# Kernel tuning notes

Measured on AMD Instinct MI355X. Metric: run time of the kernel, lower is better.

## Reference

```python
import jax, jax.numpy as jnp
import numpy as np

B, C_IN, H, W = 4, 256, 32, 32
NH, DK, DV, C_OUT = 8, 256, 256, 512
DKH = DK // NH
DVH = DV // NH


def _rel_to_abs(x):
    # x: [b, n, L, 2L-1] -> [b, n, L, L] via the pad/reshape skewing trick
    b, n, L, _ = x.shape
    x = jnp.pad(x, ((0, 0), (0, 0), (0, 0), (0, 1)))          # [b,n,L,2L]
    flat = x.reshape(b, n, L * 2 * L)
    flat = jnp.pad(flat, ((0, 0), (0, 0), (0, L - 1)))
    final = flat.reshape(b, n, L + 1, 2 * L - 1)
    return final[:, :, :L, L - 1:]


def _relative_logits_1d(q5, rel_k, Hq, Wq, perm):
    # q5: [b, nh, dkh, Hq, Wq]; rel_k: [2*Wq-1, dkh]
    b = q5.shape[0]
    rel = jnp.einsum('bhdxy,md->bhxym', q5, rel_k)            # [b,nh,Hq,Wq,2Wq-1]
    rel = rel.reshape(b, NH * Hq, Wq, 2 * Wq - 1)
    rel = _rel_to_abs(rel)                                     # [b,nh*Hq,Wq,Wq]
    rel = rel.reshape(b, NH, Hq, Wq, Wq)
    rel = jnp.broadcast_to(rel[:, :, :, None], (b, NH, Hq, Hq, Wq, Wq))
    rel = jnp.transpose(rel, perm)                             # -> [b,nh,H,W,H,W]
    return rel.reshape(b, NH, Hq * Wq, Hq * Wq)


def _forward(x, w_qkv, b_qkv, w_attn, b_attn, w_out, b_out, key_rel_h, key_rel_w):
    b = x.shape[0]
    L = H * W
    # 1x1 conv projections expressed as einsum
    qkv = jnp.einsum('bchw,oc->bohw', x, w_qkv) + b_qkv[None, :, None, None]
    q, k, v = qkv[:, :DK], qkv[:, DK:2 * DK], qkv[:, 2 * DK:]
    q = q.reshape(b, NH, DKH, L) * (DKH ** -0.5)
    k = k.reshape(b, NH, DKH, L)
    v = v.reshape(b, NH, DVH, L)
    logits = jnp.einsum('bhdl,bhdm->bhlm', q, k)              # [b,nh,L,L]
    q5 = q.reshape(b, NH, DKH, H, W)
    rel_w = _relative_logits_1d(q5, key_rel_w, H, W, (0, 1, 2, 4, 3, 5))
    rel_h = _relative_logits_1d(jnp.transpose(q5, (0, 1, 2, 4, 3)),
                                key_rel_h, W, H, (0, 1, 4, 2, 5, 3))
    logits = logits + rel_h + rel_w
    weights = jax.nn.softmax(logits, axis=-1)
    attn = jnp.einsum('bhlm,bhdm->bhdl', weights, v).reshape(b, DV, H, W)
    attn = jnp.einsum('bchw,oc->bohw', attn, w_attn) + b_attn[None, :, None, None]
    conv_out = jnp.einsum('bchw,oc->bohw', x, w_out) + b_out[None, :, None, None]
    return jnp.concatenate([conv_out, attn], axis=1)          # [b, C_OUT, H, W]


def setup_inputs() -> dict:
    key = jax.random.key(0)
    ks = jax.random.split(key, 6)
    s = 0.05
    return {
        'x': jax.random.normal(ks[0], (B, C_IN, H, W), jnp.float32),
        'w_qkv': jax.random.normal(ks[1], (2 * DK + DV, C_IN), jnp.float32) * s,
        'b_qkv': jnp.zeros((2 * DK + DV,), jnp.float32),
        'w_attn': jax.random.normal(ks[2], (DV, DV), jnp.float32) * s,
        'b_attn': jnp.zeros((DV,), jnp.float32),
        'w_out': jax.random.normal(ks[3], (C_OUT - DV, C_IN), jnp.float32) * s,
        'b_out': jnp.zeros((C_OUT - DV,), jnp.float32),
        'key_rel_h': jax.random.normal(ks[4], (2 * H - 1, DKH), jnp.float32) * s,
        'key_rel_w': jax.random.normal(ks[5], (2 * W - 1, DKH), jnp.float32) * s,
    }


def reference(x, w_qkv, b_qkv, w_attn, b_attn, w_out, b_out, key_rel_h, key_rel_w):
    return _forward(x, w_qkv, b_qkv, w_attn, b_attn, w_out, b_out,
                    key_rel_h, key_rel_w)
```

## Files before the change

### kernel.cpp

```cpp
#include <hip/hip_runtime.h>

#define NB   4
#define CIN  256
#define L    1024
#define NH   8
#define DH   32
#define COUT 512

typedef _Float16 half8 __attribute__((ext_vector_type(8)));
typedef _Float16 half4 __attribute__((ext_vector_type(4)));
typedef float    f32x4 __attribute__((ext_vector_type(4)));

__global__ __launch_bounds__(256) void k_prep(const float* __restrict__ x, const float* __restrict__ wq,
                                              const float* __restrict__ wa, const float* __restrict__ wo,
                                              const float* __restrict__ krh, const float* __restrict__ krw,
                                              _Float16* __restrict__ xbT, _Float16* __restrict__ wqb,
                                              _Float16* __restrict__ wab, _Float16* __restrict__ wob,
                                              _Float16* __restrict__ wrel) {
    int blk = blockIdx.x;
    if (blk < 128) {
        __shared__ _Float16 T[32][264];
        int b  = blk >> 5;
        int ct = (blk >> 2) & 7;
        int lt = blk & 3;
        int c0 = ct * 32, l0 = lt * 256;
        int t = threadIdx.x;
        int wv = t >> 6, lane = t & 63;
        const float* xp = x + (size_t)b * CIN * L + l0;
        #pragma unroll
        for (int i = 0; i < 8; ++i) {
            int c = wv * 8 + i;
            float4 v = *(const float4*)(xp + (size_t)(c0 + c) * L + lane * 4);
            half4 h;
            h[0] = (_Float16)v.x; h[1] = (_Float16)v.y; h[2] = (_Float16)v.z; h[3] = (_Float16)v.w;
            *(half4*)&T[c][lane * 4] = h;
        }
        __syncthreads();
        _Float16* op = xbT + ((size_t)(b * L + l0 + t)) * CIN + c0;
        half8 o[4];
        #pragma unroll
        for (int i = 0; i < 32; ++i) ((_Float16*)o)[i] = T[i][t];
        #pragma unroll
        for (int v = 0; v < 4; ++v) *(half8*)(op + v * 8) = o[v];
    } else {
        int idx = (blk - 128) * 256 + threadIdx.x;
        int i4 = idx * 4;
        if (i4 < 768 * 256) {
            float4 v = *(const float4*)(wq + i4);
            half4 h; h[0] = (_Float16)v.x; h[1] = (_Float16)v.y; h[2] = (_Float16)v.z; h[3] = (_Float16)v.w;
            *(half4*)(wqb + i4) = h;
        }
        if (i4 < 256 * 256) {
            float4 va = *(const float4*)(wa + i4);
            half4 ha; ha[0] = (_Float16)va.x; ha[1] = (_Float16)va.y; ha[2] = (_Float16)va.z; ha[3] = (_Float16)va.w;
            *(half4*)(wab + i4) = ha;
            float4 vo = *(const float4*)(wo + i4);
            half4 ho; ho[0] = (_Float16)vo.x; ho[1] = (_Float16)vo.y; ho[2] = (_Float16)vo.z; ho[3] = (_Float16)vo.w;
            *(half4*)(wob + i4) = ho;
        }
        if (idx < 4096) {
            int half_sel = idx >> 11;
            int j = idx & 2047;
            float v = 0.f;
            if (j < 63 * 32) v = half_sel ? krw[j] : krh[j];
            wrel[idx] = (_Float16)v;
        }
    }
}

__global__ __launch_bounds__(256) void k_qkv(const _Float16* __restrict__ xbT, const _Float16* __restrict__ wqb,
                                             const float* __restrict__ bqkv,
                                             _Float16* __restrict__ qb, _Float16* __restrict__ kb,
                                             _Float16* __restrict__ vt) {
    int lane = threadIdx.x & 63, wv = threadIdx.x >> 6;
    int wid = blockIdx.x * 4 + wv;
    int b = wid / 768; int rem = wid - b * 768;
    int ot = rem >> 5, lt = rem & 31;
    int g = lane >> 4, q15 = lane & 15;
    int o0 = ot * 32, l0 = lt * 32;
    const _Float16* A0 = wqb + (size_t)(o0 + q15) * CIN + g * 8;
    const _Float16* B0 = xbT + ((size_t)(b * L + l0 + q15)) * CIN + g * 8;
    f32x4 acc00 = {0,0,0,0}, acc01 = {0,0,0,0}, acc10 = {0,0,0,0}, acc11 = {0,0,0,0};
    #pragma unroll
    for (int c0 = 0; c0 < CIN; c0 += 32) {
        half8 a0 = *(const half8*)(A0 + c0);
        half8 a1 = *(const half8*)(A0 + 16 * CIN + c0);
        half8 b0 = *(const half8*)(B0 + c0);
        half8 b1 = *(const half8*)(B0 + 16 * CIN + c0);
        acc00 = __builtin_amdgcn_mfma_f32_16x16x32_f16(a0, b0, acc00, 0, 0, 0);
        acc01 = __builtin_amdgcn_mfma_f32_16x16x32_f16(a0, b1, acc01, 0, 0, 0);
        acc10 = __builtin_amdgcn_mfma_f32_16x16x32_f16(a1, b0, acc10, 0, 0, 0);
        acc11 = __builtin_amdgcn_mfma_f32_16x16x32_f16(a1, b1, acc11, 0, 0, 0);
    }
    #pragma unroll
    for (int ai = 0; ai < 2; ++ai) {
        int obase = o0 + ai * 16 + 4 * g;
        float bs0 = bqkv[obase], bs1 = bqkv[obase + 1], bs2 = bqkv[obase + 2], bs3 = bqkv[obase + 3];
        #pragma unroll
        for (int bj = 0; bj < 2; ++bj) {
            f32x4 a = (ai == 0) ? (bj == 0 ? acc00 : acc01) : (bj == 0 ? acc10 : acc11);
            float av[4] = {a[0] + bs0, a[1] + bs1, a[2] + bs2, a[3] + bs3};
            int l = l0 + bj * 16 + q15;
            if (obase < 256) {
                int h = obase >> 5, d0 = obase & 31;
                half4 w;
                #pragma unroll
                for (int r = 0; r < 4; ++r) w[r] = (_Float16)(av[r] * 0.17677669529663689f);
                *(half4*)(qb + ((size_t)((b * NH + h) * L + l)) * DH + d0) = w;
            } else if (obase < 512) {
                int o = obase - 256; int h = o >> 5, d0 = o & 31;
                half4 w;
                #pragma unroll
                for (int r = 0; r < 4; ++r) w[r] = (_Float16)av[r];
                *(half4*)(kb + ((size_t)((b * NH + h) * L + l)) * DH + d0) = w;
            } else {
                int o = obase - 512; int h = o >> 5, d0 = o & 31;
                #pragma unroll
                for (int r = 0; r < 4; ++r)
                    vt[((size_t)((b * NH + h) * DH + d0 + r)) * L + l] = (_Float16)av[r];
            }
        }
    }
}

__global__ __launch_bounds__(256) void k_attn(const _Float16* __restrict__ qb, const _Float16* __restrict__ kb,
                                              const _Float16* __restrict__ vt, const _Float16* __restrict__ wrel,
                                              _Float16* __restrict__ attnT) {
    __shared__ float SM[4][576];
    __shared__ float RelS[128 * 16];
    int lane = threadIdx.x & 63, wv = threadIdx.x >> 6;
    int wid = blockIdx.x;
    int bh = wid >> 6;
    int qbase = (wid & 63) << 4;
    int g = lane >> 4, q15 = lane & 15;
    int l = qbase + q15;
    int rl = qbase >> 5;
    int cl = (qbase & 31) + q15;

    half8 bq = *(const half8*)(qb + ((size_t)(bh * L + l)) * DH + g * 8);
    const f32x4 zf = {0.f, 0.f, 0.f, 0.f};

    #pragma unroll
    for (int s = 0; s < 2; ++s) {
        int rr0 = 32 * wv + 16 * s;
        half8 wa = *(const half8*)(wrel + (rr0 + q15) * DH + g * 8);
        f32x4 rc = __builtin_amdgcn_mfma_f32_16x16x32_f16(wa, bq, zf, 0, 0, 0);
        #pragma unroll
        for (int r = 0; r < 4; ++r) RelS[(rr0 + 4 * g + r) * 16 + q15] = rc[r];
    }
    __syncthreads();

    float rw0[4], rw1[4];
    #pragma unroll
    for (int r = 0; r < 4; ++r) {
        rw0[r] = RelS[(95 + 4 * g + r - cl) * 16 + q15] - 4.0f;
        rw1[r] = RelS[(111 + 4 * g + r - cl) * 16 + q15] - 4.0f;
    }

    const _Float16* kbase = kb + (size_t)bh * L * DH;
    const _Float16* vbase = vt + (size_t)bh * DH * L;

    float l_run = 0.f;
    f32x4 o0 = {0.f, 0.f, 0.f, 0.f}, o1 = {0.f, 0.f, 0.f, 0.f};
    _Float16* plw = (_Float16*)&SM[wv][0] + q15 * 40;
    const _Float16* plr = (_Float16*)&SM[wv][0] + q15 * 40 + g * 8;

    for (int ch = wv * 8; ch < wv * 8 + 8; ++ch) {
        int m0 = ch * 32;
        half8 k0 = *(const half8*)(kbase + (size_t)(m0 + q15) * DH + g * 8);
        half8 k1 = *(const half8*)(kbase + (size_t)(m0 + 16 + q15) * DH + g * 8);
        f32x4 s0 = __builtin_amdgcn_mfma_f32_16x16x32_f16(k0, bq, zf, 0, 0, 0);
        f32x4 s1 = __builtin_amdgcn_mfma_f32_16x16x32_f16(k1, bq, zf, 0, 0, 0);
        float rh = RelS[(ch + 31 - rl) * 16 + q15];
        half4 w0, w1;
        #pragma unroll
        for (int r = 0; r < 4; ++r) {
            float p0 = __expf(s0[r] + rh + rw0[r]);
            float p1 = __expf(s1[r] + rh + rw1[r]);
            l_run += p0 + p1;
            w0[r] = (_Float16)p0;
            w1[r] = (_Float16)p1;
        }
        *(half4*)(plw + 4 * g) = w0;
        *(half4*)(plw + 16 + 4 * g) = w1;
        half8 pf = *(const half8*)plr;
        half8 v0 = *(const half8*)(vbase + (size_t)q15 * L + m0 + g * 8);
        half8 v1 = *(const half8*)(vbase + (size_t)(16 + q15) * L + m0 + g * 8);
        o0 = __builtin_amdgcn_mfma_f32_16x16x32_f16(v0, pf, o0, 0, 0, 0);
        o1 = __builtin_amdgcn_mfma_f32_16x16x32_f16(v1, pf, o1, 0, 0, 0);
    }
    l_run += __shfl_xor(l_run, 16, 64);
    l_run += __shfl_xor(l_run, 32, 64);

    float* cw = &SM[wv][lane * 9];
    cw[0] = l_run;
    #pragma unroll
    for (int r = 0; r < 4; ++r) { cw[1 + r] = o0[r]; cw[5 + r] = o1[r]; }
    __syncthreads();
    if (wv == 0) {
        float lsum = 0.f;
        float O[8];
        #pragma unroll
        for (int j = 0; j < 8; ++j) O[j] = 0.f;
        #pragma unroll
        for (int i = 0; i < 4; ++i) {
            const float* cr = &SM[i][lane * 9];
            lsum += cr[0];
            #pragma unroll
            for (int j = 0; j < 8; ++j) O[j] += cr[1 + j];
        }
        float inv = 1.f / lsum;
        int b = bh >> 3, h = bh & 7;
        _Float16* op = attnT + ((size_t)(b * L + l)) * CIN + h * DH;
        half4 e0, e1;
        #pragma unroll
        for (int r = 0; r < 4; ++r) { e0[r] = (_Float16)(O[r] * inv); e1[r] = (_Float16)(O[4 + r] * inv); }
        *(half4*)(op + 4 * g) = e0;
        *(half4*)(op + 16 + 4 * g) = e1;
    }
}

__global__ __launch_bounds__(256) void k_out(const _Float16* __restrict__ xbT, const _Float16* __restrict__ attnT,
                                             const _Float16* __restrict__ wob, const _Float16* __restrict__ wab,
                                             const float* __restrict__ bout, const float* __restrict__ battn,
                                             float* __restrict__ out) {
    int lane = threadIdx.x & 63, wv = threadIdx.x >> 6;
    int wid = blockIdx.x * 4 + wv;
    int b = wid >> 9; int rem = wid & 511;
    int ct = rem >> 5, lt = rem & 31;
    int g = lane >> 4, q15 = lane & 15;
    int ch0 = ct * 32, l0 = lt * 32;
    bool is_conv = ch0 < 256;
    const _Float16* A0 = (is_conv ? wob + (size_t)ch0 * CIN : wab + (size_t)(ch0 - 256) * CIN) + q15 * CIN + g * 8;
    const _Float16* B0 = (is_conv ? xbT : attnT) + ((size_t)(b * L + l0 + q15)) * CIN + g * 8;
    f32x4 acc00 = {0,0,0,0}, acc01 = {0,0,0,0}, acc10 = {0,0,0,0}, acc11 = {0,0,0,0};
    #pragma unroll
    for (int c0 = 0; c0 < CIN; c0 += 32) {
        half8 a0 = *(const half8*)(A0 + c0);
        half8 a1 = *(const half8*)(A0 + 16 * CIN + c0);
        half8 b0 = *(const half8*)(B0 + c0);
        half8 b1 = *(const half8*)(B0 + 16 * CIN + c0);
        acc00 = __builtin_amdgcn_mfma_f32_16x16x32_f16(a0, b0, acc00, 0, 0, 0);
        acc01 = __builtin_amdgcn_mfma_f32_16x16x32_f16(a0, b1, acc01, 0, 0, 0);
        acc10 = __builtin_amdgcn_mfma_f32_16x16x32_f16(a1, b0, acc10, 0, 0, 0);
        acc11 = __builtin_amdgcn_mfma_f32_16x16x32_f16(a1, b1, acc11, 0, 0, 0);
    }
    #pragma unroll
    for (int ai = 0; ai < 2; ++ai) {
        int chb = ch0 + ai * 16 + 4 * g;
        float bs[4];
        #pragma unroll
        for (int r = 0; r < 4; ++r) bs[r] = is_conv ? bout[chb + r] : battn[chb + r - 256];
        #pragma unroll
        for (int bj = 0; bj < 2; ++bj) {
            f32x4 a = (ai == 0) ? (bj == 0 ? acc00 : acc01) : (bj == 0 ? acc10 : acc11);
            int l = l0 + bj * 16 + q15;
            #pragma unroll
            for (int r = 0; r < 4; ++r)
                out[((size_t)(b * COUT + chb + r)) * L + l] = a[r] + bs[r];
        }
    }
}

extern "C" void kernel_launch(void* const* d_in, const int* in_sizes, int n_in,
                              void* d_out, int out_size, void* d_ws, size_t ws_size,
                              hipStream_t stream) {
    const float* x      = (const float*)d_in[0];
    const float* w_qkv  = (const float*)d_in[1];
    const float* b_qkv  = (const float*)d_in[2];
    const float* w_attn = (const float*)d_in[3];
    const float* b_attn = (const float*)d_in[4];
    const float* w_out  = (const float*)d_in[5];
    const float* b_out  = (const float*)d_in[6];
    const float* krh    = (const float*)d_in[7];
    const float* krw    = (const float*)d_in[8];

    char* ws = (char*)d_ws;
    _Float16* xbT  = (_Float16*)(ws);
    _Float16* wqb  = (_Float16*)(ws + 2097152);
    _Float16* wab  = (_Float16*)(ws + 2490368);
    _Float16* wob  = (_Float16*)(ws + 2621440);
    _Float16* wrel = (_Float16*)(ws + 2752512);
    _Float16* qb   = (_Float16*)(ws + 2760704);
    _Float16* kb   = (_Float16*)(ws + 4857856);
    _Float16* vt   = (_Float16*)(ws + 6955008);
    _Float16* attnT= (_Float16*)(ws + 9052160);
    float* out = (float*)d_out;

    k_prep<<<dim3(320), dim3(256), 0, stream>>>(x, w_qkv, w_attn, w_out, krh, krw,
                                                xbT, wqb, wab, wob, wrel);
    k_qkv <<<dim3(768), dim3(256), 0, stream>>>(xbT, wqb, b_qkv, qb, kb, vt);
    k_attn<<<dim3(2048), dim3(256), 0, stream>>>(qb, kb, vt, wrel, attnT);
    k_out <<<dim3(512), dim3(256), 0, stream>>>(xbT, attnT, wob, wab, b_out, b_attn, out);
}
```

Baseline: 61.57 us.

## Give each wave its own query tile instead of splitting keys across waves

Each wave now handles a separate 16-query tile over all 32 key chunks, instead of four waves sharing one query tile and splitting the key range. This drops the block-wide syncs and the cross-wave LDS reduction of partial sums and outputs, and cuts the grid from 2048 to 512 blocks. In exchange each wave computes all 128 rel-logit rows into its own LDS buffer, which raises LDS use to about 37KB per block. Each wave also runs a serial loop four times longer, so latency hiding now depends more on occupancy.

```diff
diff --git a/kernel.cpp b/kernel.cpp
--- a/kernel.cpp
+++ b/kernel.cpp
@@ -126,12 +126,12 @@
 __global__ __launch_bounds__(256) void k_attn(const _Float16* __restrict__ qb, const _Float16* __restrict__ kb,
                                               const _Float16* __restrict__ vt, const _Float16* __restrict__ wrel,
                                               _Float16* __restrict__ attnT) {
-    __shared__ float SM[4][576];
-    __shared__ float RelS[128 * 16];
+    __shared__ float RelW[4][128 * 16];
+    __shared__ _Float16 Pl[4][16][40];
     int lane = threadIdx.x & 63, wv = threadIdx.x >> 6;
     int wid = blockIdx.x;
-    int bh = wid >> 6;
-    int qbase = (wid & 63) << 4;
+    int bh = wid >> 4;
+    int qbase = ((wid & 15) * 4 + wv) << 4;
     int g = lane >> 4, q15 = lane & 15;
     int l = qbase + q15;
     int rl = qbase >> 5;
@@ -140,21 +140,21 @@
     half8 bq = *(const half8*)(qb + ((size_t)(bh * L + l)) * DH + g * 8);
     const f32x4 zf = {0.f, 0.f, 0.f, 0.f};
 
-    #pragma unroll
-    for (int s = 0; s < 2; ++s) {
-        int rr0 = 32 * wv + 16 * s;
+    float* Rp = &RelW[wv][0];
+    #pragma unroll
+    for (int s = 0; s < 8; ++s) {
+        int rr0 = 16 * s;
         half8 wa = *(const half8*)(wrel + (rr0 + q15) * DH + g * 8);
         f32x4 rc = __builtin_amdgcn_mfma_f32_16x16x32_f16(wa, bq, zf, 0, 0, 0);
         #pragma unroll
-        for (int r = 0; r < 4; ++r) RelS[(rr0 + 4 * g + r) * 16 + q15] = rc[r];
-    }
-    __syncthreads();
+        for (int r = 0; r < 4; ++r) Rp[(rr0 + 4 * g + r) * 16 + q15] = rc[r];
+    }
 
     float rw0[4], rw1[4];
     #pragma unroll
     for (int r = 0; r < 4; ++r) {
-        rw0[r] = RelS[(95 + 4 * g + r - cl) * 16 + q15] - 4.0f;
-        rw1[r] = RelS[(111 + 4 * g + r - cl) * 16 + q15] - 4.0f;
+        rw0[r] = Rp[(95 + 4 * g + r - cl) * 16 + q15] - 4.0f;
+        rw1[r] = Rp[(111 + 4 * g + r - cl) * 16 + q15] - 4.0f;
     }
 
     const _Float16* kbase = kb + (size_t)bh * L * DH;
@@ -162,16 +162,16 @@
 
     float l_run = 0.f;
     f32x4 o0 = {0.f, 0.f, 0.f, 0.f}, o1 = {0.f, 0.f, 0.f, 0.f};
-    _Float16* plw = (_Float16*)&SM[wv][0] + q15 * 40;
-    const _Float16* plr = (_Float16*)&SM[wv][0] + q15 * 40 + g * 8;
-
-    for (int ch = wv * 8; ch < wv * 8 + 8; ++ch) {
+    _Float16* plw = &Pl[wv][q15][0];
+    const _Float16* plr = &Pl[wv][q15][g * 8];
+
+    for (int ch = 0; ch < 32; ++ch) {
         int m0 = ch * 32;
         half8 k0 = *(const half8*)(kbase + (size_t)(m0 + q15) * DH + g * 8);
         half8 k1 = *(const half8*)(kbase + (size_t)(m0 + 16 + q15) * DH + g * 8);
         f32x4 s0 = __builtin_amdgcn_mfma_f32_16x16x32_f16(k0, bq, zf, 0, 0, 0);
         f32x4 s1 = __builtin_amdgcn_mfma_f32_16x16x32_f16(k1, bq, zf, 0, 0, 0);
-        float rh = RelS[(ch + 31 - rl) * 16 + q15];
+        float rh = Rp[(ch + 31 - rl) * 16 + q15];
         half4 w0, w1;
         #pragma unroll
         for (int r = 0; r < 4; ++r) {
@@ -191,33 +191,15 @@
     }
     l_run += __shfl_xor(l_run, 16, 64);
     l_run += __shfl_xor(l_run, 32, 64);
-
-    float* cw = &SM[wv][lane * 9];
-    cw[0] = l_run;
-    #pragma unroll
-    for (int r = 0; r < 4; ++r) { cw[1 + r] = o0[r]; cw[5 + r] = o1[r]; }
-    __syncthreads();
-    if (wv == 0) {
-        float lsum = 0.f;
-        float O[8];
-        #pragma unroll
-        for (int j = 0; j < 8; ++j) O[j] = 0.f;
-        #pragma unroll
-        for (int i = 0; i < 4; ++i) {
-            const float* cr = &SM[i][lane * 9];
-            lsum += cr[0];
-            #pragma unroll
-            for (int j = 0; j < 8; ++j) O[j] += cr[1 + j];
-        }
-        float inv = 1.f / lsum;
-        int b = bh >> 3, h = bh & 7;
-        _Float16* op = attnT + ((size_t)(b * L + l)) * CIN + h * DH;
-        half4 e0, e1;
-        #pragma unroll
-        for (int r = 0; r < 4; ++r) { e0[r] = (_Float16)(O[r] * inv); e1[r] = (_Float16)(O[4 + r] * inv); }
-        *(half4*)(op + 4 * g) = e0;
-        *(half4*)(op + 16 + 4 * g) = e1;
-    }
+    float inv = 1.f / l_run;
+
+    int b = bh >> 3, h = bh & 7;
+    _Float16* op = attnT + ((size_t)(b * L + l)) * CIN + h * DH;
+    half4 e0, e1;
+    #pragma unroll
+    for (int r = 0; r < 4; ++r) { e0[r] = (_Float16)(o0[r] * inv); e1[r] = (_Float16)(o1[r] * inv); }
+    *(half4*)(op + 4 * g) = e0;
+    *(half4*)(op + 16 + 4 * g) = e1;
 }
 
 __global__ __launch_bounds__(256) void k_out(const _Float16* __restrict__ xbT, const _Float16* __restrict__ attnT,
@@ -290,6 +272,6 @@
     k_prep<<<dim3(320), dim3(256), 0, stream>>>(x, w_qkv, w_attn, w_out, krh, krw,
                                                 xbT, wqb, wab, wob, wrel);
     k_qkv <<<dim3(768), dim3(256), 0, stream>>>(xbT, wqb, b_qkv, qb, kb, vt);
-    k_attn<<<dim3(2048), dim3(256), 0, stream>>>(qb, kb, vt, wrel, attnT);
+    k_attn<<<dim3(512), dim3(256), 0, stream>>>(qb, kb, vt, wrel, attnT);
     k_out <<<dim3(512), dim3(256), 0, stream>>>(xbT, attnT, wob, wab, b_out, b_attn, out);
 }
```

After: 60.97 us. No clear change (-1.0%).
